# Optimization experiments

Measured on AMD Instinct MI355X. Metric: run time of the kernel, lower is better.

Reference implementation:

```python
import jax, jax.numpy as jnp
import numpy as np
from jax import lax

T, B, H_IN, H_HID = 2048, 64, 256, 256


def _orth(key, shape):
    a = jax.random.normal(key, shape, jnp.float32)
    if shape[0] >= shape[1]:
        q, _ = jnp.linalg.qr(a)
    else:
        q, _ = jnp.linalg.qr(a.T)
        q = q.T
    return q[: shape[0], : shape[1]].astype(jnp.float32)


def setup_inputs() -> dict:
    key = jax.random.key(0)
    ks = jax.random.split(key, 6)
    x = jax.random.normal(ks[0], (T, B, H_IN), jnp.float32)
    rnn_hxs = jax.random.normal(ks[1], (1, B, H_HID), jnp.float32)
    batch_mask = jax.random.randint(ks[2], (T, B), 0, 2).astype(bool)
    # force column 0 fully valid so pad_packed max length == T (static shape)
    batch_mask = batch_mask.at[:, 0].set(True)
    w_ih = _orth(ks[3], (3 * H_HID, H_IN))   # [3H, H_in] gates r,z,n
    w_hh = _orth(ks[4], (3 * H_HID, H_HID))
    b_ih = jnp.zeros((3 * H_HID,), jnp.float32)  # constant_(0) init
    b_hh = jnp.zeros((3 * H_HID,), jnp.float32)
    return {"x": x, "rnn_hxs": rnn_hxs, "batch_mask": batch_mask,
            "w_ih": w_ih, "w_hh": w_hh, "b_ih": b_ih, "b_hh": b_hh}


def _gru_ragged(x, h0, batch_mask, w_ih, w_hh, b_ih, b_hh):
    Tn, Bn, _ = x.shape
    Hh = h0.shape[-1]
    mask = batch_mask
    lens = mask.sum(0)                      # [B] per-column valid lengths
    # --- gather/pack: move valid steps of each column to the front ---
    rank = jnp.cumsum(mask, axis=0) - mask  # compact position per (t,b)
    rank_m = jnp.where(mask, rank, Tn)      # invalid rows -> dump row Tn
    cols = jnp.broadcast_to(jnp.arange(Bn), (Tn, Bn))
    compact = jnp.zeros((Tn + 1, Bn, x.shape[-1]), x.dtype)
    compact = compact.at[rank_m, cols].set(x)[:Tn]
    # --- GRU over compact sequences; h frozen past each column's length ---
    gi = jnp.einsum('tbi,gi->tbg', compact, w_ih) + b_ih  # [T,B,3H]
    valid = jnp.arange(Tn)[:, None] < lens[None, :]       # [T,B]

    def step(h, inp):
        gi_t, v = inp
        gh = jnp.einsum('bh,gh->bg', h, w_hh) + b_hh
        r = jax.nn.sigmoid(gi_t[:, :Hh] + gh[:, :Hh])
        z = jax.nn.sigmoid(gi_t[:, Hh:2 * Hh] + gh[:, Hh:2 * Hh])
        n = jnp.tanh(gi_t[:, 2 * Hh:] + r * gh[:, 2 * Hh:])
        h_new = (1.0 - z) * n + z * h
        h_out = jnp.where(v[:, None], h_new, h)
        out = jnp.where(v[:, None], h_new, 0.0)  # pad_packed zero padding
        return h_out, out

    hT, scores = lax.scan(step, h0, (gi, valid))  # scores [T,B,Hh]
    # --- masked_scatter: true positions of dest (row-major t,b order)
    # consume consecutive H-rows of the flattened padded scores ---
    mflat = mask.reshape(-1)
    flat_rank = jnp.cumsum(mflat) - mflat            # exclusive cumsum
    src = scores.reshape(Tn * Bn, Hh)
    gathered = src[flat_rank]                        # [T*B, Hh]
    out = jnp.where(mflat[:, None], gathered, 0.0).reshape(Tn, Bn, Hh)
    return out, hT


def reference(x, rnn_hxs, batch_mask, w_ih, w_hh, b_ih, b_hh):
    scores, hT = _gru_ragged(x, rnn_hxs[0], batch_mask, w_ih, w_hh, b_ih, b_hh)
    return scores, hT[None]
```

## Files before the change

kernel.cpp:

```cpp
#include <hip/hip_runtime.h>
#include <cstdint>
#include <cstddef>

#define T_LEN 2048
#define B_N   64
#define H_INP 256
#define H_HID 256
#define G3    768
#define M_ROWS (T_LEN * B_N)
#define SCH   8

typedef _Float16 f16;
typedef _Float16 f16x2 __attribute__((ext_vector_type(2)));
typedef _Float16 f16x8 __attribute__((ext_vector_type(8)));
typedef float    f32x4 __attribute__((ext_vector_type(4)));

static __device__ __forceinline__ float fdot2f(uint32_t a, uint32_t b, float c) {
#if __has_builtin(__builtin_amdgcn_fdot2)
  return __builtin_amdgcn_fdot2(__builtin_bit_cast(f16x2, a),
                                __builtin_bit_cast(f16x2, b), c, false);
#else
  f16x2 av = __builtin_bit_cast(f16x2, a);
  f16x2 bv = __builtin_bit_cast(f16x2, b);
  return c + (float)av.x * (float)bv.x + (float)av.y * (float)bv.y;
#endif
}

template <int CTRL>
static __device__ __forceinline__ float dppf(float v) {
  return __builtin_bit_cast(float,
      __builtin_amdgcn_update_dpp(0, __builtin_bit_cast(int, v), CTRL, 0xf, 0xf, true));
}
static __device__ __forceinline__ float x4sel(float v, bool hi4) {
  float lo = dppf<0x104>(v);
  float hi = dppf<0x114>(v);
  return hi4 ? hi : lo;
}
static __device__ __forceinline__ float mrg4(float lo, float hi, bool h) {
  float mine = h ? hi : lo;
  float th   = h ? lo : hi;
  return mine + x4sel(th, h);
}
static __device__ __forceinline__ float mrg2(float lo, float hi, bool h) {
  float mine = h ? hi : lo;
  float th   = h ? lo : hi;
  return mine + dppf<0x4E>(th);
}
static __device__ __forceinline__ float mrg1(float lo, float hi, bool h) {
  float mine = h ? hi : lo;
  float th   = h ? lo : hi;
  return mine + dppf<0xB1>(th);
}

static __device__ __forceinline__ void gldl16(const void* g, void* ldsbase, void* ldsexact) {
#if __has_builtin(__builtin_amdgcn_global_load_lds)
  __builtin_amdgcn_global_load_lds((const __attribute__((address_space(1))) void*)g,
                                   (__attribute__((address_space(3))) void*)ldsbase, 16, 0, 0);
  (void)ldsexact;
#else
  *(uint4*)ldsexact = *(const uint4*)g;
#endif
}

__global__ void k_zero(float4* __restrict__ p, int n4) {
  int i = blockIdx.x * blockDim.x + threadIdx.x;
  int stride = gridDim.x * blockDim.x;
  float4 z; z.x = z.y = z.z = z.w = 0.f;
  for (; i < n4; i += stride) p[i] = z;
}

__global__ void k_cvt(const float2* __restrict__ s, f16x2* __restrict__ d, int n2) {
  int i = blockIdx.x * blockDim.x + threadIdx.x;
  int stride = gridDim.x * blockDim.x;
  for (; i < n2; i += stride) {
    float2 v = s[i];
    f16x2 p; p.x = (f16)v.x; p.y = (f16)v.y;
    d[i] = p;
  }
}

__global__ __launch_bounds__(64) void k_prep_col(const int* __restrict__ mask,
                                                 unsigned short* __restrict__ tidx,
                                                 int* __restrict__ lens) {
  const int b = blockIdx.x;
  const int lane = threadIdx.x;
  unsigned short* tp = tidx + b * T_LEN;
  int base = 0;
  for (int c = 0; c < T_LEN / 64; ++c) {
    int t = c * 64 + lane;
    bool m = mask[t * B_N + b] != 0;
    unsigned long long bal = __ballot(m);
    int pc = __popcll(bal & ((1ull << lane) - 1ull));
    if (m) tp[base + pc] = (unsigned short)t;
    base += __popcll(bal);
  }
  if (lane == 0) lens[b] = base;
}

__global__ __launch_bounds__(256) void k_rowcnt(const int* __restrict__ mask,
                                                int* __restrict__ rowcnt) {
  int g = blockIdx.x * 256 + threadIdx.x;
  int t = g >> 6, lane = g & 63;
  bool m = mask[t * B_N + lane] != 0;
  unsigned long long bal = __ballot(m);
  if (lane == 0) rowcnt[t] = __popcll(bal);
}

__global__ __launch_bounds__(512) void k_rowpref(const int* __restrict__ rowcnt,
                                                 int* __restrict__ rowpref,
                                                 int* __restrict__ ntru) {
  const int tid = threadIdx.x;
  const int lane = tid & 63, w = tid >> 6;
  int4 v = ((const int4*)rowcnt)[tid];
  int s = v.x + v.y + v.z + v.w;
  int incl = s;
  for (int d = 1; d < 64; d <<= 1) {
    int t = __shfl_up(incl, d, 64);
    if (lane >= d) incl += t;
  }
  __shared__ int wt[8], wo[8];
  if (lane == 63) wt[w] = incl;
  __syncthreads();
  if (tid == 0) {
    int run = 0;
    for (int i = 0; i < 8; ++i) { wo[i] = run; run += wt[i]; }
    ntru[0] = run;
  }
  __syncthreads();
  int base = wo[w] + incl - s;
  int4 o; o.x = base; o.y = base + v.x; o.z = o.y + v.y; o.w = o.z + v.z;
  ((int4*)rowpref)[tid] = o;
}

__global__ __launch_bounds__(256) void k_inv(const int* __restrict__ mask,
                                             const int* __restrict__ rowpref,
                                             int* __restrict__ inv) {
  int g = blockIdx.x * 256 + threadIdx.x;
  int t = g >> 6, lane = g & 63;
  bool m = mask[t * B_N + lane] != 0;
  unsigned long long bal = __ballot(m);
  int r = rowpref[t] + __popcll(bal & ((1ull << lane) - 1ull));
  if (m) inv[r] = t * B_N + lane;
}

__global__ __launch_bounds__(256) void k_invT(const int* __restrict__ inv,
                                              const int* __restrict__ ntru,
                                              int* __restrict__ invT) {
  int j = blockIdx.x * 256 + threadIdx.x;
  int v = (j < ntru[0]) ? inv[j] : -1;
  invT[(j & 63) * T_LEN + (j >> 6)] = v;
}

__global__ __launch_bounds__(256) void k_gemm(const f16* __restrict__ X,
                                              const f16* __restrict__ W,
                                              const float* __restrict__ bias,
                                              f16* __restrict__ GI) {
  const int lane = threadIdx.x & 63;
  const int wave = threadIdx.x >> 6;
  const int m0 = blockIdx.x * 64 + wave * 16;
  const int n0 = blockIdx.y * 64;
  const int idx16 = lane & 15;
  const int kofs  = (lane >> 4) * 8;

  __shared__ __align__(16) f16 st[4][16][72];

  const f16* ap  = X + (size_t)(m0 + idx16) * H_INP + kofs;
  const f16* bp0 = W + (size_t)(n0 + idx16) * H_INP + kofs;

  f32x4 acc[4] = { {0,0,0,0}, {0,0,0,0}, {0,0,0,0}, {0,0,0,0} };
#pragma unroll
  for (int kt = 0; kt < 8; ++kt) {
    f16x8 a = *(const f16x8*)(ap + kt * 32);
#pragma unroll
    for (int nt = 0; nt < 4; ++nt) {
      f16x8 bb = *(const f16x8*)(bp0 + (size_t)nt * 16 * H_INP + kt * 32);
      acc[nt] = __builtin_amdgcn_mfma_f32_16x16x32_f16(a, bb, acc[nt], 0, 0, 0);
    }
  }
#pragma unroll
  for (int nt = 0; nt < 4; ++nt) {
    const int col = nt * 16 + idx16;
    const float bv = bias[n0 + col];
#pragma unroll
    for (int r = 0; r < 4; ++r)
      st[wave][(lane >> 4) * 4 + r][col] = (f16)(acc[nt][r] + bv);
  }
  {
    const int row = lane >> 2, seg = lane & 3;
    const uint4* sp = (const uint4*)&st[wave][row][seg * 16];
    uint4 v0 = sp[0], v1 = sp[1];
    uint4* gp = (uint4*)(GI + (size_t)(m0 + row) * G3 + n0 + seg * 16);
    gp[0] = v0; gp[1] = v1;
  }
}

__global__ __launch_bounds__(512)
__attribute__((amdgpu_waves_per_eu(2, 2)))
void k_scan(const f16* __restrict__ Whh,
            const f16* __restrict__ GI,
            const float* __restrict__ h0,
            const float* __restrict__ bhh,
            const unsigned short* __restrict__ tidx,
            const int* __restrict__ lens,
            const int* __restrict__ invT,
            float* __restrict__ out) {
  const int b = blockIdx.x;
  const int tid = threadIdx.x;
  const int o = tid & 7;
  const int grp = tid >> 3;
  const int rbase = grp * 12;
  const bool o4 = (tid & 4) != 0, o2 = (tid & 2) != 0, o1 = (tid & 1) != 0;

  __shared__ __align__(16) f16 GIbuf[2][SCH * G3];
  __shared__ float    outb[SCH * H_HID];
  __shared__ float    ghs[G3];
  __shared__ uint32_t hpad[160];
  __shared__ unsigned short tcol[T_LEN];
  __shared__ int      invcol[T_LEN];

  const int L = lens[b];

  uint4 wq[12][4];
#pragma unroll
  for (int i = 0; i < 12; ++i) {
    const uint4* wp = (const uint4*)(Whh + (size_t)(rbase + i) * H_HID + 32 * o);
#pragma unroll
    for (int q = 0; q < 4; ++q) wq[i][q] = wp[q];
  }
  const int rowA = rbase + o;
  const int rowB = rbase + 8 + ((tid & 4) >> 1) + ((tid & 2) >> 1);
  const float bA = bhh[rowA];
  const float bB = bhh[rowB];

  for (int i = tid; i < T_LEN; i += 512) {
    tcol[i] = tidx[b * T_LEN + i];
    invcol[i] = invT[b * T_LEN + i];
  }
  float h_reg = 0.f;
  if (tid < H_HID) {
    h_reg = h0[b * H_HID + tid];
    ((f16*)hpad)[40 * (tid >> 5) + (tid & 31)] = (f16)h_reg;
  }
  __syncthreads();

  const char* GIc = (const char*)GI;
  const int wavbase = (tid >> 6) << 10;

  auto issue_chunk = [&](int m) {
    {
      int p = tid << 4;
      int r = p / 1536;
      int kk = m * SCH + r;
      int t = tcol[kk < L ? kk : 0] & (T_LEN - 1);
      const char* src = GIc + ((size_t)((t << 6) + b)) * 1536 + (p - r * 1536);
      char* dbase = (char*)GIbuf[m & 1] + wavbase;
      gldl16(src, dbase, (char*)GIbuf[m & 1] + p);
    }
    if (tid < 256) {
      int p = 8192 + (tid << 4);
      int r = p / 1536;
      int kk = m * SCH + r;
      int t = tcol[kk < L ? kk : 0] & (T_LEN - 1);
      const char* src = GIc + ((size_t)((t << 6) + b)) * 1536 + (p - r * 1536);
      char* dbase = (char*)GIbuf[m & 1] + 8192 + wavbase;
      gldl16(src, dbase, (char*)GIbuf[m & 1] + p);
    }
  };

  issue_chunk(0);

  const int nchunks = (L + SCH - 1) >> 3;
  for (int n = 0; n < nchunks; ++n) {
    const int par = n & 1;
    if (n + 1 < nchunks) issue_chunk(n + 1);
    if (n > 0) {
      int r = tid >> 6, c4 = (tid & 63) << 2;
      int kk = (n - 1) * SCH + r;
      if (kk < L) {
        int iv = invcol[kk];
        if (iv >= 0)
          *(float4*)(out + (size_t)iv * H_HID + c4) = *(const float4*)(outb + r * H_HID + c4);
      }
    }

    const int kbase = n * SCH;
    const int smax = (L - kbase < SCH) ? (L - kbase) : SCH;
    for (int s = 0; s < smax; ++s) {
      float aa[12];
#pragma unroll
      for (int i = 0; i < 12; ++i) aa[i] = 0.f;
#pragma unroll
      for (int q = 0; q < 4; ++q) {
        uint4 hv = *((const uint4*)(hpad + 20 * o) + q);
#pragma unroll
        for (int i = 0; i < 12; ++i) {
          aa[i] = fdot2f(wq[i][q].x, hv.x, aa[i]);
          aa[i] = fdot2f(wq[i][q].y, hv.y, aa[i]);
          aa[i] = fdot2f(wq[i][q].z, hv.z, aa[i]);
          aa[i] = fdot2f(wq[i][q].w, hv.w, aa[i]);
        }
      }
      float b0 = mrg4(aa[0], aa[4], o4);
      float b1 = mrg4(aa[1], aa[5], o4);
      float b2 = mrg4(aa[2], aa[6], o4);
      float b3 = mrg4(aa[3], aa[7], o4);
      float c0 = mrg2(b0, b2, o2);
      float c1 = mrg2(b1, b3, o2);
      float ghA = mrg1(c0, c1, o1) + bA;
      float d0 = mrg4(aa[8], aa[10], o4);
      float d1 = mrg4(aa[9], aa[11], o4);
      float e  = mrg2(d0, d1, o2);
      float ghB = e + dppf<0xB1>(e) + bB;
      ghs[rowA] = ghA;
      ghs[rowB] = ghB;
      __syncthreads();
      if (tid < H_HID) {
        const f16* gib = GIbuf[par] + s * G3;
        const float gi0 = (float)gib[tid];
        const float gi1 = (float)gib[H_HID + tid];
        const float gi2 = (float)gib[2 * H_HID + tid];
        const float ghr = ghs[tid];
        const float ghz = ghs[H_HID + tid];
        const float ghn = ghs[2 * H_HID + tid];
        const float rg = __builtin_amdgcn_rcpf(1.f + __expf(-(gi0 + ghr)));
        const float zg = __builtin_amdgcn_rcpf(1.f + __expf(-(gi1 + ghz)));
        const float xx = gi2 + rg * ghn;
        const float ng = 1.f - 2.f * __builtin_amdgcn_rcpf(1.f + __expf(2.f * xx));
        const float hn = (1.f - zg) * ng + zg * h_reg;
        h_reg = hn;
        ((f16*)hpad)[40 * (tid >> 5) + (tid & 31)] = (f16)hn;
        outb[s * H_HID + tid] = hn;
      }
      __syncthreads();
    }
  }
  if (L > 0) {
    const int nc = nchunks - 1;
    int r = tid >> 6, c4 = (tid & 63) << 2;
    int kk = nc * SCH + r;
    if (kk < L) {
      int iv = invcol[kk];
      if (iv >= 0)
        *(float4*)(out + (size_t)iv * H_HID + c4) = *(const float4*)(outb + r * H_HID + c4);
    }
  }
  if (tid < H_HID)
    out[(size_t)M_ROWS * H_HID + (size_t)b * H_HID + tid] = h_reg;
}

extern "C" void kernel_launch(void* const* d_in, const int* in_sizes, int n_in,
                              void* d_out, int out_size, void* d_ws, size_t ws_size,
                              hipStream_t stream) {
  const float* x    = (const float*)d_in[0];
  const float* h0   = (const float*)d_in[1];
  const int*   mask = (const int*)d_in[2];
  const float* wih  = (const float*)d_in[3];
  const float* whh  = (const float*)d_in[4];
  const float* bih  = (const float*)d_in[5];
  const float* bhh  = (const float*)d_in[6];
  float* out = (float*)d_out;

  char* ws = (char*)d_ws;
  f16* X16   = (f16*)(ws + 0);
  int* invT  = (int*)(ws + 0);
  f16* Wih16 = (f16*)(ws + 67108864);
  f16* Whh16 = (f16*)(ws + 67502080);
  f16* GI    = (f16*)(ws + 67895296);
  unsigned short* tidx = (unsigned short*)(ws + 269221888);
  int* rowcnt  = (int*)(ws + 269484032);
  int* rowpref = (int*)(ws + 269492224);
  int* inv   = (int*)(ws + 269746176);
  int* lens  = (int*)(ws + 270270464);
  int* ntru  = (int*)(ws + 270270720);

  hipLaunchKernelGGL(k_zero, dim3(4096), dim3(256), 0, stream,
                     (float4*)d_out, out_size / 4);
  hipLaunchKernelGGL(k_cvt, dim3(4096), dim3(256), 0, stream,
                     (const float2*)x, (f16x2*)X16, M_ROWS * H_INP / 2);
  hipLaunchKernelGGL(k_cvt, dim3(96), dim3(256), 0, stream,
                     (const float2*)wih, (f16x2*)Wih16, G3 * H_INP / 2);
  hipLaunchKernelGGL(k_cvt, dim3(96), dim3(256), 0, stream,
                     (const float2*)whh, (f16x2*)Whh16, G3 * H_INP / 2);
  hipLaunchKernelGGL(k_prep_col, dim3(B_N), dim3(64), 0, stream,
                     mask, tidx, lens);
  hipLaunchKernelGGL(k_rowcnt, dim3(512), dim3(256), 0, stream, mask, rowcnt);
  hipLaunchKernelGGL(k_rowpref, dim3(1), dim3(512), 0, stream,
                     rowcnt, rowpref, ntru);
  hipLaunchKernelGGL(k_inv, dim3(512), dim3(256), 0, stream,
                     mask, rowpref, inv);
  hipLaunchKernelGGL(k_gemm, dim3(M_ROWS / 64, G3 / 64), dim3(256), 0, stream,
                     X16, Wih16, bih, GI);
  hipLaunchKernelGGL(k_invT, dim3(512), dim3(256), 0, stream,
                     inv, ntru, invT);
  hipLaunchKernelGGL(k_scan, dim3(B_N), dim3(512), 0, stream,
                     Whh16, GI, h0, bhh, tidx, lens, invT, out);
}
```

Before: 3.160 ms.

## Use MFMA for recurrent matvec in GRU scan with 256-thread blocks

Replaces the fdot2-based per-step hidden matvec with MFMA 16x16x32 f16 instructions, keeping W_hh in registers as MFMA A-fragments and broadcasting h as the B operand. This removes the DPP cross-lane reduction tree. Blocks shrink from 512 to 256 threads. Hidden state and output staging are double-buffered so each step needs only one barrier instead of two. The cost is that most of the MFMA output columns are wasted, since only column 0 is stored, and register pressure rises to 96 f16x8 fragments per thread.

```diff
diff --git a/kernel.cpp b/kernel.cpp
--- a/kernel.cpp
+++ b/kernel.cpp
@@ -14,43 +14,6 @@
 typedef _Float16 f16x2 __attribute__((ext_vector_type(2)));
 typedef _Float16 f16x8 __attribute__((ext_vector_type(8)));
 typedef float    f32x4 __attribute__((ext_vector_type(4)));
-
-static __device__ __forceinline__ float fdot2f(uint32_t a, uint32_t b, float c) {
-#if __has_builtin(__builtin_amdgcn_fdot2)
-  return __builtin_amdgcn_fdot2(__builtin_bit_cast(f16x2, a),
-                                __builtin_bit_cast(f16x2, b), c, false);
-#else
-  f16x2 av = __builtin_bit_cast(f16x2, a);
-  f16x2 bv = __builtin_bit_cast(f16x2, b);
-  return c + (float)av.x * (float)bv.x + (float)av.y * (float)bv.y;
-#endif
-}
-
-template <int CTRL>
-static __device__ __forceinline__ float dppf(float v) {
-  return __builtin_bit_cast(float,
-      __builtin_amdgcn_update_dpp(0, __builtin_bit_cast(int, v), CTRL, 0xf, 0xf, true));
-}
-static __device__ __forceinline__ float x4sel(float v, bool hi4) {
-  float lo = dppf<0x104>(v);
-  float hi = dppf<0x114>(v);
-  return hi4 ? hi : lo;
-}
-static __device__ __forceinline__ float mrg4(float lo, float hi, bool h) {
-  float mine = h ? hi : lo;
-  float th   = h ? lo : hi;
-  return mine + x4sel(th, h);
-}
-static __device__ __forceinline__ float mrg2(float lo, float hi, bool h) {
-  float mine = h ? hi : lo;
-  float th   = h ? lo : hi;
-  return mine + dppf<0x4E>(th);
-}
-static __device__ __forceinline__ float mrg1(float lo, float hi, bool h) {
-  float mine = h ? hi : lo;
-  float th   = h ? lo : hi;
-  return mine + dppf<0xB1>(th);
-}
 
 static __device__ __forceinline__ void gldl16(const void* g, void* ldsbase, void* ldsexact) {
 #if __has_builtin(__builtin_amdgcn_global_load_lds)
@@ -194,8 +157,8 @@
   }
 }
 
-__global__ __launch_bounds__(512)
-__attribute__((amdgpu_waves_per_eu(2, 2)))
+__global__ __launch_bounds__(256)
+__attribute__((amdgpu_waves_per_eu(1, 1)))
 void k_scan(const f16* __restrict__ Whh,
             const f16* __restrict__ GI,
             const float* __restrict__ h0,
@@ -206,146 +169,143 @@
             float* __restrict__ out) {
   const int b = blockIdx.x;
   const int tid = threadIdx.x;
-  const int o = tid & 7;
-  const int grp = tid >> 3;
-  const int rbase = grp * 12;
-  const bool o4 = (tid & 4) != 0, o2 = (tid & 2) != 0, o1 = (tid & 1) != 0;
-
-  __shared__ __align__(16) f16 GIbuf[2][SCH * G3];
-  __shared__ float    outb[SCH * H_HID];
-  __shared__ float    ghs[G3];
-  __shared__ uint32_t hpad[160];
+  const int w = tid >> 6;
+  const int lane = tid & 63;
+  const int g = lane >> 4;
+  const int c = lane & 15;
+
+  __shared__ __align__(16) f16   GIbuf[2][SCH * G3];
+  __shared__ __align__(16) float outb[2][SCH * H_HID];
+  __shared__ __align__(16) float ghs[G3];
+  __shared__ __align__(16) f16   hf[2][H_HID];
   __shared__ unsigned short tcol[T_LEN];
   __shared__ int      invcol[T_LEN];
 
   const int L = lens[b];
 
-  uint4 wq[12][4];
+  f16x8 wA[96];
 #pragma unroll
   for (int i = 0; i < 12; ++i) {
-    const uint4* wp = (const uint4*)(Whh + (size_t)(rbase + i) * H_HID + 32 * o);
-#pragma unroll
-    for (int q = 0; q < 4; ++q) wq[i][q] = wp[q];
-  }
-  const int rowA = rbase + o;
-  const int rowB = rbase + 8 + ((tid & 4) >> 1) + ((tid & 2) >> 1);
-  const float bA = bhh[rowA];
-  const float bB = bhh[rowB];
-
-  for (int i = tid; i < T_LEN; i += 512) {
+    const f16* wp = Whh + (size_t)((w + 4 * i) * 16 + c) * H_HID + g * 8;
+#pragma unroll
+    for (int kt = 0; kt < 8; ++kt)
+      wA[i * 8 + kt] = *(const f16x8*)(wp + kt * 32);
+  }
+
+  const int j = (w + 4 * g) * 16 + c;
+  const float bh0 = bhh[j];
+  const float bh1 = bhh[H_HID + j];
+  const float bh2 = bhh[2 * H_HID + j];
+
+  for (int i = tid; i < T_LEN; i += 256) {
     tcol[i] = tidx[b * T_LEN + i];
     invcol[i] = invT[b * T_LEN + i];
   }
-  float h_reg = 0.f;
-  if (tid < H_HID) {
-    h_reg = h0[b * H_HID + tid];
-    ((f16*)hpad)[40 * (tid >> 5) + (tid & 31)] = (f16)h_reg;
-  }
+  float h_reg = h0[b * H_HID + j];
+  hf[0][j] = (f16)h_reg;
   __syncthreads();
 
   const char* GIc = (const char*)GI;
-  const int wavbase = (tid >> 6) << 10;
+  const int wavbase = w << 10;
 
   auto issue_chunk = [&](int m) {
-    {
-      int p = tid << 4;
+#pragma unroll
+    for (int rnd = 0; rnd < 3; ++rnd) {
+      int p = rnd * 4096 + tid * 16;
       int r = p / 1536;
       int kk = m * SCH + r;
       int t = tcol[kk < L ? kk : 0] & (T_LEN - 1);
       const char* src = GIc + ((size_t)((t << 6) + b)) * 1536 + (p - r * 1536);
-      char* dbase = (char*)GIbuf[m & 1] + wavbase;
+      char* dbase = (char*)GIbuf[m & 1] + rnd * 4096 + wavbase;
       gldl16(src, dbase, (char*)GIbuf[m & 1] + p);
     }
-    if (tid < 256) {
-      int p = 8192 + (tid << 4);
-      int r = p / 1536;
-      int kk = m * SCH + r;
-      int t = tcol[kk < L ? kk : 0] & (T_LEN - 1);
-      const char* src = GIc + ((size_t)((t << 6) + b)) * 1536 + (p - r * 1536);
-      char* dbase = (char*)GIbuf[m & 1] + 8192 + wavbase;
-      gldl16(src, dbase, (char*)GIbuf[m & 1] + p);
-    }
   };
 
   issue_chunk(0);
+  __syncthreads();
+
+  const f32x4 z4 = {0.f, 0.f, 0.f, 0.f};
 
   const int nchunks = (L + SCH - 1) >> 3;
   for (int n = 0; n < nchunks; ++n) {
     const int par = n & 1;
     if (n + 1 < nchunks) issue_chunk(n + 1);
     if (n > 0) {
-      int r = tid >> 6, c4 = (tid & 63) << 2;
+      int r = tid >> 5, c8 = (tid & 31) << 3;
       int kk = (n - 1) * SCH + r;
       if (kk < L) {
         int iv = invcol[kk];
-        if (iv >= 0)
-          *(float4*)(out + (size_t)iv * H_HID + c4) = *(const float4*)(outb + r * H_HID + c4);
+        if (iv >= 0) {
+          const float* sb = &outb[par ^ 1][r * H_HID + c8];
+          float* gp = out + (size_t)iv * H_HID + c8;
+          *(float4*)gp = *(const float4*)sb;
+          *(float4*)(gp + 4) = *(const float4*)(sb + 4);
+        }
       }
     }
 
     const int kbase = n * SCH;
     const int smax = (L - kbase < SCH) ? (L - kbase) : SCH;
     for (int s = 0; s < smax; ++s) {
-      float aa[12];
-#pragma unroll
-      for (int i = 0; i < 12; ++i) aa[i] = 0.f;
-#pragma unroll
-      for (int q = 0; q < 4; ++q) {
-        uint4 hv = *((const uint4*)(hpad + 20 * o) + q);
-#pragma unroll
-        for (int i = 0; i < 12; ++i) {
-          aa[i] = fdot2f(wq[i][q].x, hv.x, aa[i]);
-          aa[i] = fdot2f(wq[i][q].y, hv.y, aa[i]);
-          aa[i] = fdot2f(wq[i][q].z, hv.z, aa[i]);
-          aa[i] = fdot2f(wq[i][q].w, hv.w, aa[i]);
+      const int rd = (kbase + s) & 1;
+      f16x8 bf[8];
+#pragma unroll
+      for (int kt = 0; kt < 8; ++kt)
+        bf[kt] = *(const f16x8*)(&hf[rd][kt * 32 + g * 8]);
+#pragma unroll
+      for (int half = 0; half < 2; ++half) {
+        f32x4 acc[6];
+#pragma unroll
+        for (int i = 0; i < 6; ++i)
+          acc[i] = __builtin_amdgcn_mfma_f32_16x16x32_f16(
+              wA[(half * 6 + i) * 8], bf[0], z4, 0, 0, 0);
+#pragma unroll
+        for (int kt = 1; kt < 8; ++kt)
+#pragma unroll
+          for (int i = 0; i < 6; ++i)
+            acc[i] = __builtin_amdgcn_mfma_f32_16x16x32_f16(
+                wA[(half * 6 + i) * 8 + kt], bf[kt], acc[i], 0, 0, 0);
+        if (c == 0) {
+#pragma unroll
+          for (int i = 0; i < 6; ++i)
+            *(f32x4*)(&ghs[(w + 4 * (half * 6 + i)) * 16 + g * 4]) = acc[i];
         }
       }
-      float b0 = mrg4(aa[0], aa[4], o4);
-      float b1 = mrg4(aa[1], aa[5], o4);
-      float b2 = mrg4(aa[2], aa[6], o4);
-      float b3 = mrg4(aa[3], aa[7], o4);
-      float c0 = mrg2(b0, b2, o2);
-      float c1 = mrg2(b1, b3, o2);
-      float ghA = mrg1(c0, c1, o1) + bA;
-      float d0 = mrg4(aa[8], aa[10], o4);
-      float d1 = mrg4(aa[9], aa[11], o4);
-      float e  = mrg2(d0, d1, o2);
-      float ghB = e + dppf<0xB1>(e) + bB;
-      ghs[rowA] = ghA;
-      ghs[rowB] = ghB;
-      __syncthreads();
-      if (tid < H_HID) {
+      {
         const f16* gib = GIbuf[par] + s * G3;
-        const float gi0 = (float)gib[tid];
-        const float gi1 = (float)gib[H_HID + tid];
-        const float gi2 = (float)gib[2 * H_HID + tid];
-        const float ghr = ghs[tid];
-        const float ghz = ghs[H_HID + tid];
-        const float ghn = ghs[2 * H_HID + tid];
+        const float gi0 = (float)gib[j];
+        const float gi1 = (float)gib[H_HID + j];
+        const float gi2 = (float)gib[2 * H_HID + j];
+        const float ghr = ghs[j] + bh0;
+        const float ghz = ghs[H_HID + j] + bh1;
+        const float ghn = ghs[2 * H_HID + j] + bh2;
         const float rg = __builtin_amdgcn_rcpf(1.f + __expf(-(gi0 + ghr)));
         const float zg = __builtin_amdgcn_rcpf(1.f + __expf(-(gi1 + ghz)));
         const float xx = gi2 + rg * ghn;
         const float ng = 1.f - 2.f * __builtin_amdgcn_rcpf(1.f + __expf(2.f * xx));
         const float hn = (1.f - zg) * ng + zg * h_reg;
         h_reg = hn;
-        ((f16*)hpad)[40 * (tid >> 5) + (tid & 31)] = (f16)hn;
-        outb[s * H_HID + tid] = hn;
+        hf[rd ^ 1][j] = (f16)hn;
+        outb[par][s * H_HID + j] = hn;
       }
       __syncthreads();
     }
   }
   if (L > 0) {
     const int nc = nchunks - 1;
-    int r = tid >> 6, c4 = (tid & 63) << 2;
+    int r = tid >> 5, c8 = (tid & 31) << 3;
     int kk = nc * SCH + r;
     if (kk < L) {
       int iv = invcol[kk];
-      if (iv >= 0)
-        *(float4*)(out + (size_t)iv * H_HID + c4) = *(const float4*)(outb + r * H_HID + c4);
-    }
-  }
-  if (tid < H_HID)
-    out[(size_t)M_ROWS * H_HID + (size_t)b * H_HID + tid] = h_reg;
+      if (iv >= 0) {
+        const float* sb = &outb[nc & 1][r * H_HID + c8];
+        float* gp = out + (size_t)iv * H_HID + c8;
+        *(float4*)gp = *(const float4*)sb;
+        *(float4*)(gp + 4) = *(const float4*)(sb + 4);
+      }
+    }
+  }
+  out[(size_t)M_ROWS * H_HID + (size_t)b * H_HID + j] = h_reg;
 }
 
 extern "C" void kernel_launch(void* const* d_in, const int* in_sizes, int n_in,
@@ -392,6 +352,6 @@
                      X16, Wih16, bih, GI);
   hipLaunchKernelGGL(k_invT, dim3(512), dim3(256), 0, stream,
                      inv, ntru, invT);
-  hipLaunchKernelGGL(k_scan, dim3(B_N), dim3(512), 0, stream,
+  hipLaunchKernelGGL(k_scan, dim3(B_N), dim3(256), 0, stream,
                      Whh16, GI, h0, bhh, tidx, lens, invT, out);
 }
```

After: 3.801 ms. 20.3% more time.

## Split recurrent matvec between MFMA and dot2 paths, one barrier per step

Applied to the files above, without the earlier changes.

The per-step W_hh·h product is split. The r/z gate rows (512) still use register-resident fdot2 with DPP reductions. The n-gate rows (256) go to v_mfma_f32_16x16x32_f16 with weights held in AGPRs. Double-buffering h (hpad/hf) and outb lets the two __syncthreads per step become a single s_waitcnt+s_barrier, and the gate update is spread across all 8 waves (32 lanes each) instead of the first 256 threads. The aim is to shorten the serial per-step latency of the recurrence, at the cost of more registers, inline asm with AGPR constraints, and a mostly empty 16-column MFMA tile.

```diff
diff --git a/kernel.cpp b/kernel.cpp
--- a/kernel.cpp
+++ b/kernel.cpp
@@ -50,6 +50,17 @@
   float mine = h ? hi : lo;
   float th   = h ? lo : hi;
   return mine + dppf<0xB1>(th);
+}
+
+static __device__ __forceinline__ void mfma_av(f32x4& d, const f16x8& a, const f16x8& b) {
+  asm("v_mfma_f32_16x16x32_f16 %0, %1, %2, %0" : "+v"(d) : "a"(a), "v"(b));
+}
+
+static __device__ __forceinline__ void step_bar() {
+  asm volatile("s_waitcnt lgkmcnt(0)\n\ts_barrier" ::: "memory");
+}
+static __device__ __forceinline__ void chunk_bar() {
+  asm volatile("s_waitcnt vmcnt(0) lgkmcnt(0)\n\ts_barrier" ::: "memory");
 }
 
 static __device__ __forceinline__ void gldl16(const void* g, void* ldsbase, void* ldsexact) {
@@ -206,45 +217,62 @@
             float* __restrict__ out) {
   const int b = blockIdx.x;
   const int tid = threadIdx.x;
-  const int o = tid & 7;
-  const int grp = tid >> 3;
-  const int rbase = grp * 12;
-  const bool o4 = (tid & 4) != 0, o2 = (tid & 2) != 0, o1 = (tid & 1) != 0;
-
-  __shared__ __align__(16) f16 GIbuf[2][SCH * G3];
-  __shared__ float    outb[SCH * H_HID];
-  __shared__ float    ghs[G3];
-  __shared__ uint32_t hpad[160];
+  const int w = tid >> 6;
+  const int lane = tid & 63;
+  const int o = lane & 7;
+  const int lg = lane >> 3;
+  const int g = lane >> 4;
+  const int c = lane & 15;
+  const bool o4 = (lane & 4) != 0, o2 = (lane & 2) != 0, o1 = (lane & 1) != 0;
+
+  __shared__ __align__(16) f16   GIbuf[2][SCH * G3];
+  __shared__ __align__(16) float outb[2][SCH * H_HID];
+  __shared__ __align__(16) float ghs[G3];
+  __shared__ __align__(16) uint32_t hpad[2][160];
+  __shared__ __align__(16) f16   hf[2][H_HID];
   __shared__ unsigned short tcol[T_LEN];
   __shared__ int      invcol[T_LEN];
 
   const int L = lens[b];
 
-  uint4 wq[12][4];
-#pragma unroll
-  for (int i = 0; i < 12; ++i) {
-    const uint4* wp = (const uint4*)(Whh + (size_t)(rbase + i) * H_HID + 32 * o);
+  const int rstart = (lg < 4) ? (32 * w + 8 * lg) : (256 + 32 * w + 8 * (lg - 4));
+  uint4 wq[8][4];
+#pragma unroll
+  for (int i = 0; i < 8; ++i) {
+    const uint4* wp = (const uint4*)(Whh + (size_t)(rstart + i) * H_HID + 32 * o);
 #pragma unroll
     for (int q = 0; q < 4; ++q) wq[i][q] = wp[q];
   }
-  const int rowA = rbase + o;
-  const int rowB = rbase + 8 + ((tid & 4) >> 1) + ((tid & 2) >> 1);
+  const int rowA = rstart + o;
   const float bA = bhh[rowA];
-  const float bB = bhh[rowB];
+
+  f16x8 wM[2][8];
+#pragma unroll
+  for (int ti = 0; ti < 2; ++ti) {
+    const f16* wp = Whh + (size_t)((32 + 2 * w + ti) * 16 + c) * H_HID + g * 8;
+#pragma unroll
+    for (int kt = 0; kt < 8; ++kt)
+      wM[ti][kt] = *(const f16x8*)(wp + kt * 32);
+  }
+
+  const int j = 32 * w + lane;
+  const float bh2 = (lane < 32) ? bhh[2 * H_HID + j] : 0.f;
 
   for (int i = tid; i < T_LEN; i += 512) {
     tcol[i] = tidx[b * T_LEN + i];
     invcol[i] = invT[b * T_LEN + i];
   }
   float h_reg = 0.f;
+  if (lane < 32) h_reg = h0[b * H_HID + j];
   if (tid < H_HID) {
-    h_reg = h0[b * H_HID + tid];
-    ((f16*)hpad)[40 * (tid >> 5) + (tid & 31)] = (f16)h_reg;
+    float hv0 = h0[b * H_HID + tid];
+    ((f16*)hpad[0])[40 * (tid >> 5) + (tid & 31)] = (f16)hv0;
+    hf[0][tid] = (f16)hv0;
   }
   __syncthreads();
 
   const char* GIc = (const char*)GI;
-  const int wavbase = (tid >> 6) << 10;
+  const int wavbase = w << 10;
 
   auto issue_chunk = [&](int m) {
     {
@@ -272,6 +300,7 @@
   const int nchunks = (L + SCH - 1) >> 3;
   for (int n = 0; n < nchunks; ++n) {
     const int par = n & 1;
+    chunk_bar();
     if (n + 1 < nchunks) issue_chunk(n + 1);
     if (n > 0) {
       int r = tid >> 6, c4 = (tid & 63) << 2;
@@ -279,59 +308,70 @@
       if (kk < L) {
         int iv = invcol[kk];
         if (iv >= 0)
-          *(float4*)(out + (size_t)iv * H_HID + c4) = *(const float4*)(outb + r * H_HID + c4);
+          *(float4*)(out + (size_t)iv * H_HID + c4) =
+              *(const float4*)(outb[par ^ 1] + r * H_HID + c4);
       }
     }
 
     const int kbase = n * SCH;
     const int smax = (L - kbase < SCH) ? (L - kbase) : SCH;
     for (int s = 0; s < smax; ++s) {
-      float aa[12];
-#pragma unroll
-      for (int i = 0; i < 12; ++i) aa[i] = 0.f;
+      const int rd = (kbase + s) & 1;
+      const f16* hfr = hf[rd] + g * 8;
+      f32x4 acc0 = {0.f, 0.f, 0.f, 0.f};
+      f32x4 acc1 = {0.f, 0.f, 0.f, 0.f};
+#pragma unroll
+      for (int kt = 0; kt < 8; ++kt) {
+        f16x8 bk = *(const f16x8*)(hfr + kt * 32);
+        mfma_av(acc0, wM[0][kt], bk);
+        mfma_av(acc1, wM[1][kt], bk);
+      }
+      float aa[8];
+#pragma unroll
+      for (int i = 0; i < 8; ++i) aa[i] = 0.f;
 #pragma unroll
       for (int q = 0; q < 4; ++q) {
-        uint4 hv = *((const uint4*)(hpad + 20 * o) + q);
-#pragma unroll
-        for (int i = 0; i < 12; ++i) {
+        uint4 hv = *((const uint4*)(hpad[rd]) + 5 * o + q);
+#pragma unroll
+        for (int i = 0; i < 8; ++i) {
           aa[i] = fdot2f(wq[i][q].x, hv.x, aa[i]);
           aa[i] = fdot2f(wq[i][q].y, hv.y, aa[i]);
           aa[i] = fdot2f(wq[i][q].z, hv.z, aa[i]);
           aa[i] = fdot2f(wq[i][q].w, hv.w, aa[i]);
         }
       }
-      float b0 = mrg4(aa[0], aa[4], o4);
-      float b1 = mrg4(aa[1], aa[5], o4);
-      float b2 = mrg4(aa[2], aa[6], o4);
-      float b3 = mrg4(aa[3], aa[7], o4);
-      float c0 = mrg2(b0, b2, o2);
-      float c1 = mrg2(b1, b3, o2);
-      float ghA = mrg1(c0, c1, o1) + bA;
-      float d0 = mrg4(aa[8], aa[10], o4);
-      float d1 = mrg4(aa[9], aa[11], o4);
-      float e  = mrg2(d0, d1, o2);
-      float ghB = e + dppf<0xB1>(e) + bB;
-      ghs[rowA] = ghA;
-      ghs[rowB] = ghB;
-      __syncthreads();
-      if (tid < H_HID) {
+      {
+        float b0 = mrg4(aa[0], aa[4], o4);
+        float b1 = mrg4(aa[1], aa[5], o4);
+        float b2 = mrg4(aa[2], aa[6], o4);
+        float b3 = mrg4(aa[3], aa[7], o4);
+        float c0 = mrg2(b0, b2, o2);
+        float c1 = mrg2(b1, b3, o2);
+        ghs[rowA] = mrg1(c0, c1, o1) + bA;
+      }
+      if (c == 0) {
+        *(f32x4*)(&ghs[512 + 32 * w + g * 4]) = acc0;
+        *(f32x4*)(&ghs[512 + 32 * w + 16 + g * 4]) = acc1;
+      }
+      if (lane < 32) {
         const f16* gib = GIbuf[par] + s * G3;
-        const float gi0 = (float)gib[tid];
-        const float gi1 = (float)gib[H_HID + tid];
-        const float gi2 = (float)gib[2 * H_HID + tid];
-        const float ghr = ghs[tid];
-        const float ghz = ghs[H_HID + tid];
-        const float ghn = ghs[2 * H_HID + tid];
+        const float gi0 = (float)gib[j];
+        const float gi1 = (float)gib[H_HID + j];
+        const float gi2 = (float)gib[2 * H_HID + j];
+        const float ghr = ghs[j];
+        const float ghz = ghs[H_HID + j];
+        const float ghn = ghs[2 * H_HID + j] + bh2;
         const float rg = __builtin_amdgcn_rcpf(1.f + __expf(-(gi0 + ghr)));
         const float zg = __builtin_amdgcn_rcpf(1.f + __expf(-(gi1 + ghz)));
         const float xx = gi2 + rg * ghn;
         const float ng = 1.f - 2.f * __builtin_amdgcn_rcpf(1.f + __expf(2.f * xx));
         const float hn = (1.f - zg) * ng + zg * h_reg;
         h_reg = hn;
-        ((f16*)hpad)[40 * (tid >> 5) + (tid & 31)] = (f16)hn;
-        outb[s * H_HID + tid] = hn;
-      }
-      __syncthreads();
+        ((f16*)hpad[rd ^ 1])[40 * w + lane] = (f16)hn;
+        hf[rd ^ 1][j] = (f16)hn;
+        outb[par][s * H_HID + j] = hn;
+      }
+      step_bar();
     }
   }
   if (L > 0) {
@@ -341,11 +381,12 @@
     if (kk < L) {
       int iv = invcol[kk];
       if (iv >= 0)
-        *(float4*)(out + (size_t)iv * H_HID + c4) = *(const float4*)(outb + r * H_HID + c4);
-    }
-  }
-  if (tid < H_HID)
-    out[(size_t)M_ROWS * H_HID + (size_t)b * H_HID + tid] = h_reg;
+        *(float4*)(out + (size_t)iv * H_HID + c4) =
+            *(const float4*)(outb[nc & 1] + r * H_HID + c4);
+    }
+  }
+  if (lane < 32)
+    out[(size_t)M_ROWS * H_HID + (size_t)b * H_HID + j] = h_reg;
 }
 
 extern "C" void kernel_launch(void* const* d_in, const int* in_sizes, int n_in,
```

Result: slower. 3.508 ms (+11.0%).

## Widen GRU scan to 768 threads with one gate row per thread and lighter barriers

Applied to the files above, without the earlier changes.

The recurrent scan block grows from 512 to 768 threads, so each thread holds 8 W_hh rows instead of 12 and writes exactly one hidden-gate value, which removes the irregular second-row reduction. Per-step __syncthreads is replaced by an LDS-only waitcnt plus s_barrier, and the global-to-LDS prefetch wait moves to a single chunk-level barrier. The hidden-state buffer is double-buffered to avoid read/write hazards under the lighter barrier. The goal is a shorter serial per-step critical path, at the cost of more waves synchronising at each barrier and a tighter register budget.

```diff
diff --git a/kernel.cpp b/kernel.cpp
--- a/kernel.cpp
+++ b/kernel.cpp
@@ -50,6 +50,13 @@
   float mine = h ? hi : lo;
   float th   = h ? lo : hi;
   return mine + dppf<0xB1>(th);
+}
+
+static __device__ __forceinline__ void step_bar() {
+  asm volatile("s_waitcnt lgkmcnt(0)\n\ts_barrier" ::: "memory");
+}
+static __device__ __forceinline__ void chunk_bar() {
+  asm volatile("s_waitcnt vmcnt(0) lgkmcnt(0)\n\ts_barrier" ::: "memory");
 }
 
 static __device__ __forceinline__ void gldl16(const void* g, void* ldsbase, void* ldsexact) {
@@ -194,8 +201,8 @@
   }
 }
 
-__global__ __launch_bounds__(512)
-__attribute__((amdgpu_waves_per_eu(2, 2)))
+__global__ __launch_bounds__(768)
+__attribute__((amdgpu_waves_per_eu(3, 3)))
 void k_scan(const f16* __restrict__ Whh,
             const f16* __restrict__ GI,
             const float* __restrict__ h0,
@@ -208,38 +215,34 @@
   const int tid = threadIdx.x;
   const int o = tid & 7;
   const int grp = tid >> 3;
-  const int rbase = grp * 12;
   const bool o4 = (tid & 4) != 0, o2 = (tid & 2) != 0, o1 = (tid & 1) != 0;
 
-  __shared__ __align__(16) f16 GIbuf[2][SCH * G3];
-  __shared__ float    outb[SCH * H_HID];
-  __shared__ float    ghs[G3];
-  __shared__ uint32_t hpad[160];
+  __shared__ __align__(16) f16   GIbuf[2][SCH * G3];
+  __shared__ __align__(16) float outb[SCH * H_HID];
+  __shared__ __align__(16) float ghs[G3];
+  __shared__ __align__(16) uint32_t hpad[2][160];
   __shared__ unsigned short tcol[T_LEN];
   __shared__ int      invcol[T_LEN];
 
   const int L = lens[b];
 
-  uint4 wq[12][4];
-#pragma unroll
-  for (int i = 0; i < 12; ++i) {
-    const uint4* wp = (const uint4*)(Whh + (size_t)(rbase + i) * H_HID + 32 * o);
+  uint4 wq[8][4];
+#pragma unroll
+  for (int i = 0; i < 8; ++i) {
+    const uint4* wp = (const uint4*)(Whh + (size_t)(8 * grp + i) * H_HID + 32 * o);
 #pragma unroll
     for (int q = 0; q < 4; ++q) wq[i][q] = wp[q];
   }
-  const int rowA = rbase + o;
-  const int rowB = rbase + 8 + ((tid & 4) >> 1) + ((tid & 2) >> 1);
-  const float bA = bhh[rowA];
-  const float bB = bhh[rowB];
-
-  for (int i = tid; i < T_LEN; i += 512) {
+  const float bA = bhh[tid];
+
+  for (int i = tid; i < T_LEN; i += 768) {
     tcol[i] = tidx[b * T_LEN + i];
     invcol[i] = invT[b * T_LEN + i];
   }
   float h_reg = 0.f;
   if (tid < H_HID) {
     h_reg = h0[b * H_HID + tid];
-    ((f16*)hpad)[40 * (tid >> 5) + (tid & 31)] = (f16)h_reg;
+    ((f16*)hpad[0])[40 * (tid >> 5) + (tid & 31)] = (f16)h_reg;
   }
   __syncthreads();
 
@@ -247,24 +250,13 @@
   const int wavbase = (tid >> 6) << 10;
 
   auto issue_chunk = [&](int m) {
-    {
-      int p = tid << 4;
-      int r = p / 1536;
-      int kk = m * SCH + r;
-      int t = tcol[kk < L ? kk : 0] & (T_LEN - 1);
-      const char* src = GIc + ((size_t)((t << 6) + b)) * 1536 + (p - r * 1536);
-      char* dbase = (char*)GIbuf[m & 1] + wavbase;
-      gldl16(src, dbase, (char*)GIbuf[m & 1] + p);
-    }
-    if (tid < 256) {
-      int p = 8192 + (tid << 4);
-      int r = p / 1536;
-      int kk = m * SCH + r;
-      int t = tcol[kk < L ? kk : 0] & (T_LEN - 1);
-      const char* src = GIc + ((size_t)((t << 6) + b)) * 1536 + (p - r * 1536);
-      char* dbase = (char*)GIbuf[m & 1] + 8192 + wavbase;
-      gldl16(src, dbase, (char*)GIbuf[m & 1] + p);
-    }
+    int p = tid << 4;
+    int r = p / 1536;
+    int kk = m * SCH + r;
+    int t = tcol[kk < L ? kk : 0] & (T_LEN - 1);
+    const char* src = GIc + ((size_t)((t << 6) + b)) * 1536 + (p - r * 1536);
+    char* dbase = (char*)GIbuf[m & 1] + wavbase;
+    gldl16(src, dbase, (char*)GIbuf[m & 1] + p);
   };
 
   issue_chunk(0);
@@ -272,48 +264,47 @@
   const int nchunks = (L + SCH - 1) >> 3;
   for (int n = 0; n < nchunks; ++n) {
     const int par = n & 1;
+    chunk_bar();
     if (n + 1 < nchunks) issue_chunk(n + 1);
-    if (n > 0) {
+    if (n > 0 && tid < 512) {
       int r = tid >> 6, c4 = (tid & 63) << 2;
       int kk = (n - 1) * SCH + r;
       if (kk < L) {
         int iv = invcol[kk];
         if (iv >= 0)
-          *(float4*)(out + (size_t)iv * H_HID + c4) = *(const float4*)(outb + r * H_HID + c4);
+          *(float4*)(out + (size_t)iv * H_HID + c4) =
+              *(const float4*)(outb + r * H_HID + c4);
       }
     }
 
     const int kbase = n * SCH;
     const int smax = (L - kbase < SCH) ? (L - kbase) : SCH;
     for (int s = 0; s < smax; ++s) {
-      float aa[12];
-#pragma unroll
-      for (int i = 0; i < 12; ++i) aa[i] = 0.f;
+      const int rd = (kbase + s) & 1;
+      float aa[8];
+#pragma unroll
+      for (int i = 0; i < 8; ++i) aa[i] = 0.f;
 #pragma unroll
       for (int q = 0; q < 4; ++q) {
-        uint4 hv = *((const uint4*)(hpad + 20 * o) + q);
-#pragma unroll
-        for (int i = 0; i < 12; ++i) {
+        uint4 hv = *((const uint4*)(hpad[rd]) + 5 * o + q);
+#pragma unroll
+        for (int i = 0; i < 8; ++i) {
           aa[i] = fdot2f(wq[i][q].x, hv.x, aa[i]);
           aa[i] = fdot2f(wq[i][q].y, hv.y, aa[i]);
           aa[i] = fdot2f(wq[i][q].z, hv.z, aa[i]);
           aa[i] = fdot2f(wq[i][q].w, hv.w, aa[i]);
         }
       }
-      float b0 = mrg4(aa[0], aa[4], o4);
-      float b1 = mrg4(aa[1], aa[5], o4);
-      float b2 = mrg4(aa[2], aa[6], o4);
-      float b3 = mrg4(aa[3], aa[7], o4);
-      float c0 = mrg2(b0, b2, o2);
-      float c1 = mrg2(b1, b3, o2);
-      float ghA = mrg1(c0, c1, o1) + bA;
-      float d0 = mrg4(aa[8], aa[10], o4);
-      float d1 = mrg4(aa[9], aa[11], o4);
-      float e  = mrg2(d0, d1, o2);
-      float ghB = e + dppf<0xB1>(e) + bB;
-      ghs[rowA] = ghA;
-      ghs[rowB] = ghB;
-      __syncthreads();
+      {
+        float b0 = mrg4(aa[0], aa[4], o4);
+        float b1 = mrg4(aa[1], aa[5], o4);
+        float b2 = mrg4(aa[2], aa[6], o4);
+        float b3 = mrg4(aa[3], aa[7], o4);
+        float c0 = mrg2(b0, b2, o2);
+        float c1 = mrg2(b1, b3, o2);
+        ghs[tid] = mrg1(c0, c1, o1) + bA;
+      }
+      step_bar();
       if (tid < H_HID) {
         const f16* gib = GIbuf[par] + s * G3;
         const float gi0 = (float)gib[tid];
@@ -328,20 +319,21 @@
         const float ng = 1.f - 2.f * __builtin_amdgcn_rcpf(1.f + __expf(2.f * xx));
         const float hn = (1.f - zg) * ng + zg * h_reg;
         h_reg = hn;
-        ((f16*)hpad)[40 * (tid >> 5) + (tid & 31)] = (f16)hn;
+        ((f16*)hpad[rd ^ 1])[40 * (tid >> 5) + (tid & 31)] = (f16)hn;
         outb[s * H_HID + tid] = hn;
       }
-      __syncthreads();
+      step_bar();
     }
   }
-  if (L > 0) {
+  if (L > 0 && tid < 512) {
     const int nc = nchunks - 1;
     int r = tid >> 6, c4 = (tid & 63) << 2;
     int kk = nc * SCH + r;
     if (kk < L) {
       int iv = invcol[kk];
       if (iv >= 0)
-        *(float4*)(out + (size_t)iv * H_HID + c4) = *(const float4*)(outb + r * H_HID + c4);
+        *(float4*)(out + (size_t)iv * H_HID + c4) =
+            *(const float4*)(outb + r * H_HID + c4);
     }
   }
   if (tid < H_HID)
@@ -392,6 +384,6 @@
                      X16, Wih16, bih, GI);
   hipLaunchKernelGGL(k_invT, dim3(512), dim3(256), 0, stream,
                      inv, ntru, invT);
-  hipLaunchKernelGGL(k_scan, dim3(B_N), dim3(512), 0, stream,
+  hipLaunchKernelGGL(k_scan, dim3(B_N), dim3(768), 0, stream,
                      Whh16, GI, h0, bhh, tidx, lens, invT, out);
 }
```

Measured after the change: 3.227 ms. 1.02x slower.
